# Kernel optimization log

Measured on AMD Instinct MI355X. Metric: run time of the kernel, lower is better.

## Reference

```python
import jax, jax.numpy as jnp
import numpy as np

DIM_MODEL = 2048
H, DK, DV, L = 16, 128, 128, 2048
LN_EPS = 1e-5


def setup_inputs() -> dict:
    key = jax.random.key(0)
    ks = jax.random.split(key, 8)
    # xavier-ish scale for weights so softmax logits stay sane
    w_scale = (2.0 / (DIM_MODEL + DK)) ** 0.5
    q = jax.random.normal(ks[0], (1, L, DIM_MODEL), dtype=jnp.float32)
    k = jax.random.normal(ks[1], (1, L, DIM_MODEL), dtype=jnp.float32)
    v = jax.random.normal(ks[2], (1, L, DIM_MODEL), dtype=jnp.float32)
    Wq = jax.random.normal(ks[3], (H, DIM_MODEL, DK), dtype=jnp.float32) * w_scale
    Wk = jax.random.normal(ks[4], (H, DIM_MODEL, DK), dtype=jnp.float32) * w_scale
    Wv = jax.random.normal(ks[5], (H, DIM_MODEL, DV), dtype=jnp.float32) * w_scale
    proj_w = jax.random.normal(ks[6], (H * DV, DIM_MODEL), dtype=jnp.float32) * (1.0 / (H * DV) ** 0.5)
    proj_b = jnp.zeros((DIM_MODEL,), dtype=jnp.float32)
    ln_g = jnp.ones((DIM_MODEL,), dtype=jnp.float32)
    ln_b = jnp.zeros((DIM_MODEL,), dtype=jnp.float32)
    return {"q": q, "k": k, "v": v, "Wq": Wq, "Wk": Wk, "Wv": Wv,
            "proj_w": proj_w, "proj_b": proj_b, "ln_g": ln_g, "ln_b": ln_b}


def reference(q, k, v, Wq, Wk, Wv, proj_w, proj_b, ln_g, ln_b):
    # batch must be 1 (enforced by torch.bmm shape rules in the source)
    residual = q  # (1, L, D)
    qs, kv, vv = q[0], k[0], v[0]  # (L, D)
    dim_model = qs.shape[-1]
    temper = jnp.asarray(dim_model, qs.dtype) ** 0.5  # sqrt(dim_model), NOT sqrt(dk)
    qh = jnp.einsum('ld,hdk->hlk', qs, Wq)  # (H, L, dk)
    kh = jnp.einsum('ld,hdk->hlk', kv, Wk)  # (H, L, dk)
    vh = jnp.einsum('ld,hdv->hlv', vv, Wv)  # (H, L, dv)
    scores = jnp.einsum('hqk,hmk->hqm', qh, kh) / temper  # (H, Lq, Lk)
    # faithful quirk: softmax over dim=1 (the QUERY axis)
    attn = jax.nn.softmax(scores, axis=1)
    # attn_dropout / dropout are identity in eval mode
    out = jnp.einsum('hqm,hmv->hqv', attn, vh)  # (H, Lq, dv)
    # cat(split(out, batch=1, dim=0), dim=-1) == move head axis into features
    Lq = out.shape[1]
    out = jnp.transpose(out, (1, 0, 2)).reshape(Lq, -1)  # (Lq, H*dv)
    out = out @ proj_w + proj_b  # (Lq, dim_model)
    y = out[None] + residual  # (1, Lq, D)
    mu = jnp.mean(y, axis=-1, keepdims=True)
    var = jnp.mean((y - mu) ** 2, axis=-1, keepdims=True)
    y = (y - mu) * jax.lax.rsqrt(var + LN_EPS) * ln_g + ln_b
    return (y, attn)
```

## Files before the change

kernel.cpp:

```cpp
#include <hip/hip_runtime.h>
#include <stdint.h>

#define L 2048
#define DMODEL 2048
#define NH 16

typedef __bf16 bf16x8 __attribute__((ext_vector_type(8)));
typedef float f32x4 __attribute__((ext_vector_type(4)));
typedef short s16x4 __attribute__((ext_vector_type(4)));

__device__ __forceinline__ unsigned short f2bf(float f) {
    union { float f; unsigned int i; } w; w.f = f;
    unsigned int u = w.i;
    unsigned int r = u + 0x7fffu + ((u >> 16) & 1u);
    return (unsigned short)(r >> 16);
}

__device__ __forceinline__ void gload_lds16(const unsigned short* g, unsigned short* l) {
    __builtin_amdgcn_global_load_lds(
        (const __attribute__((address_space(1))) void*)g,
        (__attribute__((address_space(3))) void*)l, 16, 0, 0);
}

template<int CMODE, int BM, int BK, int PSM>
__global__ __launch_bounds__(256, 2)
void gemm_bt(const unsigned short* __restrict__ Ag,
             const unsigned short* __restrict__ B,
             void* __restrict__ C,
             int K, int lda, int ldb, int ldc,
             long long sA, long long sB, long long sC, float alpha,
             float* __restrict__ pPart)
{
    constexpr int KC8 = BK / 8;
    constexpr int CA  = BM * BK / 2048;
    constexpr int CB  = BK / 16;
    constexpr int MFR = BM / 32;
    constexpr int KG  = BK / 32;

    __shared__ unsigned short As[2][BM * BK];
    __shared__ unsigned short Bs[2][128 * BK];

    const int tid  = threadIdx.x;
    const int wave = tid >> 6;
    const int lane = tid & 63;
    const int quad = lane >> 4;
    const int l16  = lane & 15;

    const int tileN = blockIdx.x * 128;
    const int tileM = blockIdx.y * BM;

    const long long zA = (CMODE == 3) ? (long long)(blockIdx.z >> 4) : (long long)blockIdx.z;
    const unsigned short* A16 = Ag + zA * sA;
    B += (long long)blockIdx.z * sB;

    const int wm = (wave >> 1) * (BM / 2);
    const int wn = (wave & 1) * 64;

    auto stageB = [&](int kk, int buf) {
        #pragma unroll
        for (int j = 0; j < CB; ++j) {
            const int ch = tid + j * 256;
            const int rb = ch / KC8, kb = (ch % KC8) * 8;
            gload_lds16(B + (long long)(tileN + rb) * ldb + (kk + kb), &Bs[buf][ch * 8]);
        }
    };
    auto stageA = [&](int kk, int buf) {
        #pragma unroll
        for (int j = 0; j < CA; ++j) {
            const int ch = tid + j * 256;
            const int ra = ch / KC8, ka = (ch % KC8) * 8;
            gload_lds16(A16 + (long long)(tileM + ra) * lda + (kk + ka), &As[buf][ch * 8]);
        }
    };

    f32x4 acc[MFR][4] = {};
    const int nt = K / BK;

    stageA(0, 0);
    stageB(0, 0);
    __syncthreads();

    int cur = 0;
    for (int t = 0; t < nt; ++t) {
        const int nxt = cur ^ 1;
        const int k0n = (t + 1) * BK;
        if (t + 1 < nt) { stageA(k0n, nxt); stageB(k0n, nxt); }

        bf16x8 af[MFR][KG], bfr[4][KG];
        #pragma unroll
        for (int i = 0; i < MFR; ++i)
            #pragma unroll
            for (int g = 0; g < KG; ++g)
                af[i][g] = *(const bf16x8*)(&As[cur][(wm + i * 16 + l16) * BK + g * 32 + quad * 8]);
        #pragma unroll
        for (int j = 0; j < 4; ++j)
            #pragma unroll
            for (int g = 0; g < KG; ++g)
                bfr[j][g] = *(const bf16x8*)(&Bs[cur][(wn + j * 16 + l16) * BK + g * 32 + quad * 8]);
        #pragma unroll
        for (int g = 0; g < KG; ++g)
            #pragma unroll
            for (int i = 0; i < MFR; ++i)
                #pragma unroll
                for (int j = 0; j < 4; ++j)
                    acc[i][j] = __builtin_amdgcn_mfma_f32_16x16x32_bf16(af[i][g], bfr[j][g], acc[i][j], 0, 0, 0);

        __syncthreads();
        cur = nxt;
    }

    const long long cb = (long long)blockIdx.z * sC;
    const float aEff = (CMODE == 3) ? (blockIdx.z < 16 ? alpha : 1.0f) : alpha;
    if constexpr (CMODE != 4) {
        #pragma unroll
        for (int i = 0; i < MFR; ++i) {
            const int r0 = tileM + wm + i * 16 + quad * 4;
            #pragma unroll
            for (int j = 0; j < 4; ++j) {
                const int c = tileN + wn + j * 16 + l16;
                f32x4 d = acc[i][j];
                if (CMODE == 0) {
                    unsigned short* Cp = (unsigned short*)C + cb;
                    #pragma unroll
                    for (int r = 0; r < 4; ++r)
                        Cp[(long long)(r0 + r) * ldc + c] = f2bf(d[r] * aEff);
                } else if (CMODE == 1) {
                    unsigned short* Cp = (unsigned short*)C + cb + (long long)c * ldc + r0;
                    s16x4 pk;
                    #pragma unroll
                    for (int r = 0; r < 4; ++r) pk[r] = (short)f2bf(d[r] * aEff);
                    *(s16x4*)Cp = pk;
                } else if (CMODE == 2) {
                    float* Cp = (float*)C + cb;
                    #pragma unroll
                    for (int r = 0; r < 4; ++r)
                        Cp[(long long)(r0 + r) * ldc + c] = d[r] * aEff;
                } else {
                    if (blockIdx.z < 32) {
                        unsigned short* Cp = (unsigned short*)C + cb;
                        #pragma unroll
                        for (int r = 0; r < 4; ++r)
                            Cp[(long long)(r0 + r) * 128 + c] = f2bf(d[r] * aEff);
                    } else {
                        unsigned short* Cp = (unsigned short*)C + cb + (long long)c * 2048 + r0;
                        s16x4 pk;
                        #pragma unroll
                        for (int r = 0; r < 4; ++r) pk[r] = (short)f2bf(d[r]);
                        *(s16x4*)Cp = pk;
                    }
                }
            }
        }
    }

    if constexpr (PSM) {
        __shared__ float shPm[2][128], shPe[2][128];
        const int wmh = wave >> 1;
        #pragma unroll
        for (int j = 0; j < 4; ++j) {
            float mj = -1e30f;
            #pragma unroll
            for (int i = 0; i < MFR; ++i)
                #pragma unroll
                for (int r = 0; r < 4; ++r) mj = fmaxf(mj, acc[i][j][r]);
            float ej = 0.f;
            #pragma unroll
            for (int i = 0; i < MFR; ++i)
                #pragma unroll
                for (int r = 0; r < 4; ++r) ej += __expf(acc[i][j][r] - mj);
            #pragma unroll
            for (int off = 16; off < 64; off <<= 1) {
                float mo = __shfl_xor(mj, off, 64);
                float eo = __shfl_xor(ej, off, 64);
                float mn = fmaxf(mj, mo);
                ej = ej * __expf(mj - mn) + eo * __expf(mo - mn);
                mj = mn;
            }
            if (quad == 0) {
                shPm[wmh][wn + j * 16 + l16] = mj;
                shPe[wmh][wn + j * 16 + l16] = ej;
            }
        }
        __syncthreads();
        if (tid < 128) {
            const float mA = shPm[0][tid], mB = shPm[1][tid];
            const float m = fmaxf(mA, mB);
            const float e = shPe[0][tid] * __expf(mA - m) + shPe[1][tid] * __expf(mB - m);
            const long long pidx = ((long long)blockIdx.z * 16 + blockIdx.y) * 2048 + tileN + tid;
            pPart[pidx] = m;
            pPart[pidx + 16 * 16 * 2048] = e;
        }
    }
}

__global__ __launch_bounds__(256, 2)
void fused_pv(const unsigned short* __restrict__ qh,
              const unsigned short* __restrict__ kh,
              const unsigned short* __restrict__ vhT,
              const float* __restrict__ Mg, const float* __restrict__ iLg,
              float* __restrict__ attn, unsigned short* __restrict__ O)
{
    __shared__ unsigned short qh_s[128 * 128];
    __shared__ unsigned short kh_s[2][32 * 128];
    __shared__ unsigned short vh_s[2][128 * 32];
    __shared__ unsigned short p16[2][128 * 32];

    const int tid = threadIdx.x;
    const int wave = tid >> 6, lane = tid & 63, quad = lane >> 4, l16 = lane & 15;
    const int qt = blockIdx.x, h = blockIdx.y;
    const int wA = wave >> 1, wB = wave & 1;
    const unsigned short* qg = qh + (long long)h * 262144 + (long long)qt * 128 * 128;
    const unsigned short* kg = kh + (long long)h * 262144;
    const unsigned short* vg = vhT + (long long)h * 262144;
    const float* mgp = Mg + h * 2048;
    const float* ilp = iLg + h * 2048;
    float* ap = attn + (long long)h * L * L + (long long)qt * 128 * 2048;

    auto stage_kv = [&](int kt, int buf) {
        #pragma unroll
        for (int jj = 0; jj < 2; ++jj) {
            const int c = tid + jj * 256;
            const int rl = c >> 4, sl = (c & 15) ^ (rl & 7);
            gload_lds16(kg + (long long)(kt * 32 + rl) * 128 + sl * 8, &kh_s[buf][c * 8]);
        }
        #pragma unroll
        for (int jj = 0; jj < 2; ++jj) {
            const int c = tid + jj * 256;
            const int vd = c >> 2, sl = (c & 3) ^ (vd & 3);
            gload_lds16(vg + (long long)vd * 2048 + kt * 32 + sl * 8, &vh_s[buf][c * 8]);
        }
    };

    #pragma unroll
    for (int jj = 0; jj < 8; ++jj) {
        const int c = tid + jj * 256;
        const int rl = c >> 4, sl = (c & 15) ^ (rl & 7);
        gload_lds16(qg + (long long)rl * 128 + sl * 8, &qh_s[c * 8]);
    }
    stage_kv(0, 0);
    __syncthreads();

    f32x4 acc_o[4][4] = {};
    const int krow = wA * 16 + l16;

    for (int t = 0; t < 64; ++t) {
        const int cb = t & 1;
        if (t > 0) {
            const int pb = cb ^ 1;
            bf16x8 pa[4], vb[4];
            #pragma unroll
            for (int i = 0; i < 4; ++i) {
                const int q = wA * 64 + i * 16 + l16;
                pa[i] = *(const bf16x8*)(&p16[pb][q * 32 + ((quad * 8) ^ ((q & 3) << 3))]);
            }
            #pragma unroll
            for (int j = 0; j < 4; ++j) {
                const int vd = wB * 64 + j * 16 + l16;
                vb[j] = *(const bf16x8*)(&vh_s[pb][vd * 32 + ((quad * 8) ^ ((vd & 3) << 3))]);
            }
            #pragma unroll
            for (int i = 0; i < 4; ++i)
                #pragma unroll
                for (int j = 0; j < 4; ++j)
                    acc_o[i][j] = __builtin_amdgcn_mfma_f32_16x16x32_bf16(pa[i], vb[j], acc_o[i][j], 0, 0, 0);
        }
        __builtin_amdgcn_sched_barrier(0);
        if (t < 63) stage_kv(t + 1, cb ^ 1);

        bf16x8 af[4];
        #pragma unroll
        for (int g = 0; g < 4; ++g)
            af[g] = *(const bf16x8*)(&kh_s[cb][krow * 128 + ((g * 32 + quad * 8) ^ ((krow & 7) << 3))]);
        f32x4 acc_s[4];
        #pragma unroll
        for (int j = 0; j < 4; ++j) {
            const int q = wB * 64 + j * 16 + l16;
            f32x4 s = {};
            #pragma unroll
            for (int g = 0; g < 4; ++g) {
                bf16x8 bq = *(const bf16x8*)(&qh_s[q * 128 + ((g * 32 + quad * 8) ^ ((q & 7) << 3))]);
                s = __builtin_amdgcn_mfma_f32_16x16x32_bf16(af[g], bq, s, 0, 0, 0);
            }
            acc_s[j] = s;
        }

        const int kb = t * 32 + wA * 16 + quad * 4;
        const f32x4 mg4 = *(const f32x4*)(mgp + kb);
        const f32x4 il4 = *(const f32x4*)(ilp + kb);
        #pragma unroll
        for (int j = 0; j < 4; ++j) {
            const int q = wB * 64 + j * 16 + l16;
            f32x4 p;
            #pragma unroll
            for (int r = 0; r < 4; ++r)
                p[r] = __expf(acc_s[j][r] - mg4[r]) * il4[r];
            *(f32x4*)(ap + (long long)q * 2048 + kb) = p;
            s16x4 pk;
            #pragma unroll
            for (int r = 0; r < 4; ++r) pk[r] = (short)f2bf(p[r]);
            *(s16x4*)(&p16[cb][q * 32 + ((wA * 16 + quad * 4) ^ ((q & 3) << 3))]) = pk;
        }
        __syncthreads();
    }

    {
        bf16x8 pa[4], vb[4];
        #pragma unroll
        for (int i = 0; i < 4; ++i) {
            const int q = wA * 64 + i * 16 + l16;
            pa[i] = *(const bf16x8*)(&p16[1][q * 32 + ((quad * 8) ^ ((q & 3) << 3))]);
        }
        #pragma unroll
        for (int j = 0; j < 4; ++j) {
            const int vd = wB * 64 + j * 16 + l16;
            vb[j] = *(const bf16x8*)(&vh_s[1][vd * 32 + ((quad * 8) ^ ((vd & 3) << 3))]);
        }
        #pragma unroll
        for (int i = 0; i < 4; ++i)
            #pragma unroll
            for (int j = 0; j < 4; ++j)
                acc_o[i][j] = __builtin_amdgcn_mfma_f32_16x16x32_bf16(pa[i], vb[j], acc_o[i][j], 0, 0, 0);
    }

    #pragma unroll
    for (int i = 0; i < 4; ++i) {
        const int q = qt * 128 + wA * 64 + i * 16 + quad * 4;
        #pragma unroll
        for (int j = 0; j < 4; ++j) {
            const int vd = h * 128 + wB * 64 + j * 16 + l16;
            #pragma unroll
            for (int r = 0; r < 4; ++r)
                O[(long long)(q + r) * 2048 + vd] = f2bf(acc_o[i][j][r]);
        }
    }
}

__global__ __launch_bounds__(256)
void colstats(const float* __restrict__ pPart, float* __restrict__ Mg,
              float* __restrict__ iLg)
{
    const int c = blockIdx.x * 256 + threadIdx.x;
    const int h = blockIdx.y;
    const float* pm = pPart + (long long)h * 16 * 2048 + c;
    const float* pe = pm + 16 * 16 * 2048;
    float M = -1e30f;
    #pragma unroll
    for (int b = 0; b < 16; ++b) M = fmaxf(M, pm[b * 2048]);
    float Ls = 0.f;
    #pragma unroll
    for (int b = 0; b < 16; ++b) Ls += pe[b * 2048] * __expf(pm[b * 2048] - M);
    Mg[h * 2048 + c]  = M;
    iLg[h * 2048 + c] = 1.0f / Ls;
}

__global__ __launch_bounds__(256)
void cvt_f2b3(const float* __restrict__ a, const float* __restrict__ b,
              const float* __restrict__ c, unsigned short* __restrict__ out)
{
    const float* in = blockIdx.z == 0 ? a : blockIdx.z == 1 ? b : c;
    const long long i = ((long long)blockIdx.x * 256 + threadIdx.x) * 8;
    const float4 f0 = *(const float4*)(in + i);
    const float4 f1 = *(const float4*)(in + i + 4);
    union { int4 v; unsigned short u[8]; } t;
    t.u[0] = f2bf(f0.x); t.u[1] = f2bf(f0.y); t.u[2] = f2bf(f0.z); t.u[3] = f2bf(f0.w);
    t.u[4] = f2bf(f1.x); t.u[5] = f2bf(f1.y); t.u[6] = f2bf(f1.z); t.u[7] = f2bf(f1.w);
    *(int4*)(out + (long long)blockIdx.z * 4194304 + i) = t.v;
}

__global__ __launch_bounds__(256)
void transpose_f2b(const float* __restrict__ in, unsigned short* __restrict__ out,
                   int rows, int cols)
{
    __shared__ float t[32][33];
    const long long base = (long long)blockIdx.z * rows * cols;
    const int c0 = blockIdx.x * 32, r0 = blockIdx.y * 32;
    const int tx = threadIdx.x, ty0 = threadIdx.y;
    #pragma unroll
    for (int jj = 0; jj < 4; ++jj) {
        const int j = ty0 + jj * 8;
        t[j][tx] = in[base + (long long)(r0 + j) * cols + (c0 + tx)];
    }
    __syncthreads();
    #pragma unroll
    for (int jj = 0; jj < 4; ++jj) {
        const int j = ty0 + jj * 8;
        out[base + (long long)(c0 + j) * rows + (r0 + tx)] = f2bf(t[tx][j]);
    }
}

__global__ __launch_bounds__(256)
void transpose_f2b3(const float* __restrict__ Wq, const float* __restrict__ Wk,
                    const float* __restrict__ Wv, unsigned short* __restrict__ out)
{
    __shared__ float t[32][33];
    const int z = blockIdx.z, widx = z >> 4, h = z & 15;
    const float* in = (widx == 0 ? Wq : widx == 1 ? Wk : Wv) + (long long)h * 2048 * 128;
    unsigned short* o = out + (long long)z * 262144;
    const int c0 = blockIdx.x * 32, r0 = blockIdx.y * 32;
    const int tx = threadIdx.x, ty0 = threadIdx.y;
    #pragma unroll
    for (int jj = 0; jj < 4; ++jj) {
        const int j = ty0 + jj * 8;
        t[j][tx] = in[(long long)(r0 + j) * 128 + (c0 + tx)];
    }
    __syncthreads();
    #pragma unroll
    for (int jj = 0; jj < 4; ++jj) {
        const int j = ty0 + jj * 8;
        o[(long long)(c0 + j) * 2048 + (r0 + tx)] = f2bf(t[tx][j]);
    }
}

__global__ __launch_bounds__(256)
void ln_resid(const float* __restrict__ ypre, const float* __restrict__ resid,
              const float* __restrict__ pb, const float* __restrict__ g,
              const float* __restrict__ bta, float* __restrict__ y)
{
    __shared__ float as_[4], as2_[4];
    const int l = blockIdx.x;
    const int tid = threadIdx.x;
    float v[8]; float s = 0.f, s2 = 0.f;
    #pragma unroll
    for (int i = 0; i < 8; ++i) {
        const int d = tid + i * 256;
        float t = ypre[(long long)l * DMODEL + d] + pb[d] + resid[(long long)l * DMODEL + d];
        v[i] = t; s += t; s2 += t * t;
    }
    #pragma unroll
    for (int off = 32; off > 0; off >>= 1) {
        s  += __shfl_down(s, off, 64);
        s2 += __shfl_down(s2, off, 64);
    }
    const int wave = tid >> 6, lane = tid & 63;
    if (lane == 0) { as_[wave] = s; as2_[wave] = s2; }
    __syncthreads();
    const float S  = as_[0] + as_[1] + as_[2] + as_[3];
    const float S2 = as2_[0] + as2_[1] + as2_[2] + as2_[3];
    const float mu  = S * (1.0f / DMODEL);
    const float var = S2 * (1.0f / DMODEL) - mu * mu;
    const float rs  = rsqrtf(var + 1e-5f);
    #pragma unroll
    for (int i = 0; i < 8; ++i) {
        const int d = tid + i * 256;
        y[(long long)l * DMODEL + d] = (v[i] - mu) * rs * g[d] + bta[d];
    }
}

extern "C" void kernel_launch(void* const* d_in, const int* in_sizes, int n_in,
                              void* d_out, int out_size, void* d_ws, size_t ws_size,
                              hipStream_t stream)
{
    const float* q  = (const float*)d_in[0];
    const float* k  = (const float*)d_in[1];
    const float* v  = (const float*)d_in[2];
    const float* Wq = (const float*)d_in[3];
    const float* Wk = (const float*)d_in[4];
    const float* Wv = (const float*)d_in[5];
    const float* Pw = (const float*)d_in[6];
    const float* Pb = (const float*)d_in[7];
    const float* Lg = (const float*)d_in[8];
    const float* Lb = (const float*)d_in[9];

    float* y    = (float*)d_out;
    float* attn = y + (size_t)L * DMODEL;

    const size_t SEG = (size_t)4194304;
    unsigned short* T0  = (unsigned short*)d_ws;
    unsigned short* qh  = T0 + SEG;
    unsigned short* kh  = qh + SEG;
    unsigned short* vhT = kh + SEG;
    unsigned short* O   = vhT + SEG;
    float* ypre  = (float*)qh;
    float* pPart = (float*)d_ws;
    float* Mg    = pPart + 2 * 16 * 16 * 2048;
    float* iLg   = Mg + 16 * 2048;

    unsigned short* qkvb = (unsigned short*)attn;
    unsigned short* WT   = qkvb + 3 * SEG;

    const float inv_temper = 0.022097086912079608f;
    dim3 tb(32, 8);

    cvt_f2b3<<<dim3(2048, 1, 3), 256, 0, stream>>>(q, k, v, qkvb);
    transpose_f2b3<<<dim3(4, 64, 48), tb, 0, stream>>>(Wq, Wk, Wv, WT);

    gemm_bt<3, 128, 32, 0><<<dim3(1, 16, 48), 256, 0, stream>>>(qkvb, WT, qh,
        2048, 2048, 2048, 0, 4194304LL, 262144LL, 262144LL, inv_temper, nullptr);

    gemm_bt<4, 128, 32, 1><<<dim3(16, 16, 16), 256, 0, stream>>>(qh, kh, nullptr,
        128, 128, 128, 0, 262144LL, 262144LL, 0LL, 1.0f, pPart);

    colstats<<<dim3(8, NH), 256, 0, stream>>>(pPart, Mg, iLg);

    fused_pv<<<dim3(16, NH), 256, 0, stream>>>(qh, kh, vhT, Mg, iLg, attn, O);

    transpose_f2b<<<dim3(64, 64, 1), tb, 0, stream>>>(Pw, T0, 2048, 2048);
    gemm_bt<2, 64, 64, 0><<<dim3(16, 32, 1), 256, 0, stream>>>(O, T0, (void*)ypre,
        2048, 2048, 2048, 2048, 0LL, 0LL, 0LL, 1.0f, nullptr);

    ln_resid<<<dim3(2048), 256, 0, stream>>>(ypre, q, Pb, Lg, Lb, y);
}
```

Before: 596.7 us.

## Swizzle GEMM LDS tiles, enlarge BK, halve fused_pv query tile with triple-buffered V

Adds an XOR swizzle to the A/B shared-memory staging and fragment reads in gemm_bt so the row-strided LDS reads hit fewer bank conflicts. It also raises BK from 32 to 64 for the QKV-projection and score GEMMs. fused_pv now handles 64 query rows per block instead of 128, which doubles the grid to 512 blocks. The P·V product for each tile is computed in the same iteration after a sync, and V gets a three-deep LDS buffer. The aim is more parallelism across CUs and lower LDS pressure. The cost is re-reading K/V once per query tile, so twice as many K/V loads in total, and larger LDS tiles in the GEMMs.

After: 597.4 us. About the same (+0.1%).

```diff
diff --git a/kernel.cpp b/kernel.cpp
--- a/kernel.cpp
+++ b/kernel.cpp
@@ -32,6 +32,7 @@
              float* __restrict__ pPart)
 {
     constexpr int KC8 = BK / 8;
+    constexpr int SWM = (KC8 >= 8) ? 7 : (KC8 - 1);
     constexpr int CA  = BM * BK / 2048;
     constexpr int CB  = BK / 16;
     constexpr int MFR = BM / 32;
@@ -60,16 +61,16 @@
         #pragma unroll
         for (int j = 0; j < CB; ++j) {
             const int ch = tid + j * 256;
-            const int rb = ch / KC8, kb = (ch % KC8) * 8;
-            gload_lds16(B + (long long)(tileN + rb) * ldb + (kk + kb), &Bs[buf][ch * 8]);
+            const int rb = ch / KC8, sl = (ch % KC8) ^ (rb & SWM);
+            gload_lds16(B + (long long)(tileN + rb) * ldb + (kk + sl * 8), &Bs[buf][ch * 8]);
         }
     };
     auto stageA = [&](int kk, int buf) {
         #pragma unroll
         for (int j = 0; j < CA; ++j) {
             const int ch = tid + j * 256;
-            const int ra = ch / KC8, ka = (ch % KC8) * 8;
-            gload_lds16(A16 + (long long)(tileM + ra) * lda + (kk + ka), &As[buf][ch * 8]);
+            const int ra = ch / KC8, sl = (ch % KC8) ^ (ra & SWM);
+            gload_lds16(A16 + (long long)(tileM + ra) * lda + (kk + sl * 8), &As[buf][ch * 8]);
         }
     };
 
@@ -88,15 +89,19 @@
 
         bf16x8 af[MFR][KG], bfr[4][KG];
         #pragma unroll
-        for (int i = 0; i < MFR; ++i)
+        for (int i = 0; i < MFR; ++i) {
+            const int rr = wm + i * 16 + l16;
             #pragma unroll
             for (int g = 0; g < KG; ++g)
-                af[i][g] = *(const bf16x8*)(&As[cur][(wm + i * 16 + l16) * BK + g * 32 + quad * 8]);
-        #pragma unroll
-        for (int j = 0; j < 4; ++j)
+                af[i][g] = *(const bf16x8*)(&As[cur][rr * BK + ((g * 32 + quad * 8) ^ ((rr & SWM) << 3))]);
+        }
+        #pragma unroll
+        for (int j = 0; j < 4; ++j) {
+            const int rr = wn + j * 16 + l16;
             #pragma unroll
             for (int g = 0; g < KG; ++g)
-                bfr[j][g] = *(const bf16x8*)(&Bs[cur][(wn + j * 16 + l16) * BK + g * 32 + quad * 8]);
+                bfr[j][g] = *(const bf16x8*)(&Bs[cur][rr * BK + ((g * 32 + quad * 8) ^ ((rr & SWM) << 3))]);
+        }
         #pragma unroll
         for (int g = 0; g < KG; ++g)
             #pragma unroll
@@ -200,81 +205,62 @@
               const float* __restrict__ Mg, const float* __restrict__ iLg,
               float* __restrict__ attn, unsigned short* __restrict__ O)
 {
-    __shared__ unsigned short qh_s[128 * 128];
+    __shared__ unsigned short qh_s[64 * 128];
     __shared__ unsigned short kh_s[2][32 * 128];
-    __shared__ unsigned short vh_s[2][128 * 32];
-    __shared__ unsigned short p16[2][128 * 32];
+    __shared__ unsigned short vh_s[3][128 * 32];
+    __shared__ unsigned short p16[2][64 * 32];
 
     const int tid = threadIdx.x;
     const int wave = tid >> 6, lane = tid & 63, quad = lane >> 4, l16 = lane & 15;
     const int qt = blockIdx.x, h = blockIdx.y;
     const int wA = wave >> 1, wB = wave & 1;
-    const unsigned short* qg = qh + (long long)h * 262144 + (long long)qt * 128 * 128;
+    const unsigned short* qg = qh + (long long)h * 262144 + (long long)qt * 64 * 128;
     const unsigned short* kg = kh + (long long)h * 262144;
     const unsigned short* vg = vhT + (long long)h * 262144;
     const float* mgp = Mg + h * 2048;
     const float* ilp = iLg + h * 2048;
-    float* ap = attn + (long long)h * L * L + (long long)qt * 128 * 2048;
-
-    auto stage_kv = [&](int kt, int buf) {
+    float* ap = attn + (long long)h * L * L + (long long)qt * 64 * 2048;
+
+    auto stage_kv = [&](int kt, int kb_, int vb_) {
         #pragma unroll
         for (int jj = 0; jj < 2; ++jj) {
             const int c = tid + jj * 256;
             const int rl = c >> 4, sl = (c & 15) ^ (rl & 7);
-            gload_lds16(kg + (long long)(kt * 32 + rl) * 128 + sl * 8, &kh_s[buf][c * 8]);
+            gload_lds16(kg + (long long)(kt * 32 + rl) * 128 + sl * 8, &kh_s[kb_][c * 8]);
         }
         #pragma unroll
         for (int jj = 0; jj < 2; ++jj) {
             const int c = tid + jj * 256;
             const int vd = c >> 2, sl = (c & 3) ^ (vd & 3);
-            gload_lds16(vg + (long long)vd * 2048 + kt * 32 + sl * 8, &vh_s[buf][c * 8]);
+            gload_lds16(vg + (long long)vd * 2048 + kt * 32 + sl * 8, &vh_s[vb_][c * 8]);
         }
     };
 
     #pragma unroll
-    for (int jj = 0; jj < 8; ++jj) {
+    for (int jj = 0; jj < 4; ++jj) {
         const int c = tid + jj * 256;
         const int rl = c >> 4, sl = (c & 15) ^ (rl & 7);
         gload_lds16(qg + (long long)rl * 128 + sl * 8, &qh_s[c * 8]);
     }
-    stage_kv(0, 0);
+    stage_kv(0, 0, 0);
     __syncthreads();
 
-    f32x4 acc_o[4][4] = {};
+    f32x4 acc_o[2][4] = {};
     const int krow = wA * 16 + l16;
 
     for (int t = 0; t < 64; ++t) {
         const int cb = t & 1;
-        if (t > 0) {
-            const int pb = cb ^ 1;
-            bf16x8 pa[4], vb[4];
-            #pragma unroll
-            for (int i = 0; i < 4; ++i) {
-                const int q = wA * 64 + i * 16 + l16;
-                pa[i] = *(const bf16x8*)(&p16[pb][q * 32 + ((quad * 8) ^ ((q & 3) << 3))]);
-            }
-            #pragma unroll
-            for (int j = 0; j < 4; ++j) {
-                const int vd = wB * 64 + j * 16 + l16;
-                vb[j] = *(const bf16x8*)(&vh_s[pb][vd * 32 + ((quad * 8) ^ ((vd & 3) << 3))]);
-            }
-            #pragma unroll
-            for (int i = 0; i < 4; ++i)
-                #pragma unroll
-                for (int j = 0; j < 4; ++j)
-                    acc_o[i][j] = __builtin_amdgcn_mfma_f32_16x16x32_bf16(pa[i], vb[j], acc_o[i][j], 0, 0, 0);
-        }
-        __builtin_amdgcn_sched_barrier(0);
-        if (t < 63) stage_kv(t + 1, cb ^ 1);
+        const int vb3 = t % 3;
+        if (t < 63) stage_kv(t + 1, cb ^ 1, (t + 1) % 3);
 
         bf16x8 af[4];
         #pragma unroll
         for (int g = 0; g < 4; ++g)
             af[g] = *(const bf16x8*)(&kh_s[cb][krow * 128 + ((g * 32 + quad * 8) ^ ((krow & 7) << 3))]);
-        f32x4 acc_s[4];
-        #pragma unroll
-        for (int j = 0; j < 4; ++j) {
-            const int q = wB * 64 + j * 16 + l16;
+        f32x4 acc_s[2];
+        #pragma unroll
+        for (int j = 0; j < 2; ++j) {
+            const int q = wB * 32 + j * 16 + l16;
             f32x4 s = {};
             #pragma unroll
             for (int g = 0; g < 4; ++g) {
@@ -288,8 +274,8 @@
         const f32x4 mg4 = *(const f32x4*)(mgp + kb);
         const f32x4 il4 = *(const f32x4*)(ilp + kb);
         #pragma unroll
-        for (int j = 0; j < 4; ++j) {
-            const int q = wB * 64 + j * 16 + l16;
+        for (int j = 0; j < 2; ++j) {
+            const int q = wB * 32 + j * 16 + l16;
             f32x4 p;
             #pragma unroll
             for (int r = 0; r < 4; ++r)
@@ -300,31 +286,30 @@
             for (int r = 0; r < 4; ++r) pk[r] = (short)f2bf(p[r]);
             *(s16x4*)(&p16[cb][q * 32 + ((wA * 16 + quad * 4) ^ ((q & 3) << 3))]) = pk;
         }
+
         __syncthreads();
-    }
-
-    {
-        bf16x8 pa[4], vb[4];
-        #pragma unroll
-        for (int i = 0; i < 4; ++i) {
-            const int q = wA * 64 + i * 16 + l16;
-            pa[i] = *(const bf16x8*)(&p16[1][q * 32 + ((quad * 8) ^ ((q & 3) << 3))]);
+
+        bf16x8 pa[2], vb[4];
+        #pragma unroll
+        for (int i = 0; i < 2; ++i) {
+            const int qq = wA * 32 + i * 16 + l16;
+            pa[i] = *(const bf16x8*)(&p16[cb][qq * 32 + ((quad * 8) ^ ((qq & 3) << 3))]);
         }
         #pragma unroll
         for (int j = 0; j < 4; ++j) {
             const int vd = wB * 64 + j * 16 + l16;
-            vb[j] = *(const bf16x8*)(&vh_s[1][vd * 32 + ((quad * 8) ^ ((vd & 3) << 3))]);
-        }
-        #pragma unroll
-        for (int i = 0; i < 4; ++i)
+            vb[j] = *(const bf16x8*)(&vh_s[vb3][vd * 32 + ((quad * 8) ^ ((vd & 3) << 3))]);
+        }
+        #pragma unroll
+        for (int i = 0; i < 2; ++i)
             #pragma unroll
             for (int j = 0; j < 4; ++j)
                 acc_o[i][j] = __builtin_amdgcn_mfma_f32_16x16x32_bf16(pa[i], vb[j], acc_o[i][j], 0, 0, 0);
     }
 
     #pragma unroll
-    for (int i = 0; i < 4; ++i) {
-        const int q = qt * 128 + wA * 64 + i * 16 + quad * 4;
+    for (int i = 0; i < 2; ++i) {
+        const int q = qt * 64 + wA * 32 + i * 16 + quad * 4;
         #pragma unroll
         for (int j = 0; j < 4; ++j) {
             const int vd = h * 128 + wB * 64 + j * 16 + l16;
@@ -484,15 +469,15 @@
     cvt_f2b3<<<dim3(2048, 1, 3), 256, 0, stream>>>(q, k, v, qkvb);
     transpose_f2b3<<<dim3(4, 64, 48), tb, 0, stream>>>(Wq, Wk, Wv, WT);
 
-    gemm_bt<3, 128, 32, 0><<<dim3(1, 16, 48), 256, 0, stream>>>(qkvb, WT, qh,
+    gemm_bt<3, 128, 64, 0><<<dim3(1, 16, 48), 256, 0, stream>>>(qkvb, WT, qh,
         2048, 2048, 2048, 0, 4194304LL, 262144LL, 262144LL, inv_temper, nullptr);
 
-    gemm_bt<4, 128, 32, 1><<<dim3(16, 16, 16), 256, 0, stream>>>(qh, kh, nullptr,
+    gemm_bt<4, 128, 64, 1><<<dim3(16, 16, 16), 256, 0, stream>>>(qh, kh, nullptr,
         128, 128, 128, 0, 262144LL, 262144LL, 0LL, 1.0f, pPart);
 
     colstats<<<dim3(8, NH), 256, 0, stream>>>(pPart, Mg, iLg);
 
-    fused_pv<<<dim3(16, NH), 256, 0, stream>>>(qh, kh, vhT, Mg, iLg, attn, O);
+    fused_pv<<<dim3(32, NH), 256, 0, stream>>>(qh, kh, vhT, Mg, iLg, attn, O);
 
     transpose_f2b<<<dim3(64, 64, 1), tb, 0, stream>>>(Pw, T0, 2048, 2048);
     gemm_bt<2, 64, 64, 0><<<dim3(16, 32, 1), 256, 0, stream>>>(O, T0, (void*)ypre,
```
